# Optimization experiments

Measured on AMD Instinct MI355X. Metric: run time of the kernel, lower is better.

## Reference

```python
import jax, jax.numpy as jnp
import numpy as np

N_HEADS = 16
HEAD_SIZE = 64
SEQ_LEN = 2048
EMBED = 1024
BATCH = 2


def setup_inputs() -> dict:
    key = jax.random.key(0)
    ks = jax.random.split(key, 9)
    d_inner = N_HEADS * HEAD_SIZE
    s = 1.0 / np.sqrt(EMBED)
    inp = {
        "inputs": jax.random.normal(ks[0], (BATCH, SEQ_LEN, EMBED), jnp.float32),
        "Wq": jax.random.uniform(ks[1], (EMBED, d_inner), jnp.float32, -s, s),
        "bq": jax.random.uniform(ks[2], (d_inner,), jnp.float32, -s, s),
        "Wk": jax.random.uniform(ks[3], (EMBED, d_inner), jnp.float32, -s, s),
        "bk": jax.random.uniform(ks[4], (d_inner,), jnp.float32, -s, s),
        "Wv": jax.random.uniform(ks[5], (EMBED, d_inner), jnp.float32, -s, s),
        "bv": jax.random.uniform(ks[6], (d_inner,), jnp.float32, -s, s),
        "Wo": jax.random.uniform(ks[7], (d_inner, EMBED), jnp.float32, -s, s),
        "bo": jax.random.uniform(ks[8], (EMBED,), jnp.float32, -s, s),
    }
    return inp


def reference(inputs, Wq, bq, Wk, bk, Wv, bv, Wo, bo):
    B, S, _ = inputs.shape
    # QKV projections -> [B, H, S, Dh]
    def proj(W, b):
        return (inputs @ W + b).reshape(B, S, N_HEADS, HEAD_SIZE).transpose(0, 2, 1, 3)
    q, k, v = proj(Wq, bq), proj(Wk, bk), proj(Wv, bv)
    scores = jnp.einsum("bhqd,bhkd->bhqk", q, k) / jnp.sqrt(jnp.float32(HEAD_SIZE))
    causal = jnp.tril(jnp.ones((S, S), dtype=bool))  # [S, S]
    scores = jnp.where(causal[None, None], scores, -jnp.inf)
    attn = jax.nn.softmax(scores, axis=-1)  # dropout is identity in eval
    out = jnp.einsum("bhqk,bhkd->bhqd", attn, v)
    out = out.transpose(0, 2, 1, 3).reshape(B, S, N_HEADS * HEAD_SIZE)
    return out @ Wo + bo
```

## Files before the change

kernel.cpp:

```cpp
#include <hip/hip_runtime.h>
#include <hip/hip_bf16.h>
#include <math.h>

#define NH 16
#define DH 64
#define SEQ 2048
#define EMBED 1024
#define DINNER 1024
#define BATCH 2
#define MTOK 4096

typedef __bf16 bf16x8 __attribute__((ext_vector_type(8)));
typedef float  f32x4  __attribute__((ext_vector_type(4)));
typedef float  f32x16 __attribute__((ext_vector_type(16)));
typedef unsigned int u32;

__device__ __forceinline__ void gload16(const void* g, void* l) {
    __builtin_amdgcn_global_load_lds((const __attribute__((address_space(1))) void*)g,
                                     (__attribute__((address_space(3))) void*)l, 16, 0, 0);
}

__global__ __launch_bounds__(256) void cvt_bf16(
    const float* __restrict__ src, __bf16* __restrict__ dst, int n)
{
    int i = (blockIdx.x * 256 + threadIdx.x) * 4;
    if (i + 3 < n) {
        float4 v = *(const float4*)&src[i];
        dst[i + 0] = (__bf16)v.x;
        dst[i + 1] = (__bf16)v.y;
        dst[i + 2] = (__bf16)v.z;
        dst[i + 3] = (__bf16)v.w;
    }
}

__global__ __launch_bounds__(256) void tconv4(
    const float* __restrict__ W0, const float* __restrict__ W1,
    const float* __restrict__ W2, const float* __restrict__ W3,
    __bf16* __restrict__ D0, __bf16* __restrict__ D1,
    __bf16* __restrict__ D2, __bf16* __restrict__ D3)
{
    const int z = blockIdx.z;
    const float* __restrict__ src = (z == 0) ? W0 : (z == 1) ? W1 : (z == 2) ? W2 : W3;
    __bf16* __restrict__ dst      = (z == 0) ? D0 : (z == 1) ? D1 : (z == 2) ? D2 : D3;
    const int R = 1024, C = 1024;

    __shared__ float t[32][33];
    const int c0 = blockIdx.x * 32, r0 = blockIdx.y * 32;
    const int x = threadIdx.x & 31, y = threadIdx.x >> 5;
#pragma unroll
    for (int i = 0; i < 4; ++i)
        t[y + 8 * i][x] = src[(size_t)(r0 + y + 8 * i) * C + c0 + x];
    __syncthreads();
#pragma unroll
    for (int i = 0; i < 4; ++i)
        dst[(size_t)(c0 + y + 8 * i) * R + r0 + x] = (__bf16)t[x][y + 8 * i];
}

#define QSCALE 0.18033688f

__global__ __launch_bounds__(512) void gemm128(
    const __bf16* __restrict__ A,
    const __bf16* __restrict__ Bt0, const __bf16* __restrict__ Bt1, const __bf16* __restrict__ Bt2,
    const float* __restrict__ b0, const float* __restrict__ b1, const float* __restrict__ b2,
    void* __restrict__ o0, void* __restrict__ o1, void* __restrict__ o2,
    int Kdim, int mode3)
{
    const int z = blockIdx.z;
    const __bf16* __restrict__ Bt = (z == 0) ? Bt0 : (z == 1) ? Bt1 : Bt2;
    const float*  __restrict__ bias = (z == 0) ? b0 : (z == 1) ? b1 : b2;
    void* __restrict__ outp = (z == 0) ? o0 : (z == 1) ? o1 : o2;
    const int mode = mode3 ? 3 : z;

    __shared__ __bf16 As[128 * 32];
    __shared__ __bf16 Bs[128 * 32];

    const int tid  = threadIdx.x;
    const int lane = tid & 63;
    const int wid  = tid >> 6;
    const int wm = wid >> 1, wn = wid & 1;
    const int ls = lane & 15, lg = lane >> 4;
    const int m0 = blockIdx.y * 128, n0 = blockIdx.x * 128;

    const int sr = tid >> 2;
    const int sc = (tid & 3) * 8;

    f32x4 acc[2][4] = {};

    for (int k0 = 0; k0 < Kdim; k0 += 32) {
        gload16(&A [(size_t)(m0 + sr) * Kdim + k0 + sc], &As[sr * 32 + sc]);
        gload16(&Bt[(size_t)(n0 + sr) * Kdim + k0 + sc], &Bs[sr * 32 + sc]);
        __syncthreads();

        bf16x8 af[2], bfr[4];
#pragma unroll
        for (int i = 0; i < 2; ++i)
            af[i] = *(const bf16x8*)&As[(wm * 32 + i * 16 + ls) * 32 + lg * 8];
#pragma unroll
        for (int jx = 0; jx < 4; ++jx)
            bfr[jx] = *(const bf16x8*)&Bs[(wn * 64 + jx * 16 + ls) * 32 + lg * 8];
#pragma unroll
        for (int i = 0; i < 2; ++i)
#pragma unroll
            for (int jx = 0; jx < 4; ++jx)
                acc[i][jx] = __builtin_amdgcn_mfma_f32_16x16x32_bf16(af[i], bfr[jx], acc[i][jx], 0, 0, 0);
        __syncthreads();
    }

#pragma unroll
    for (int i = 0; i < 2; ++i) {
#pragma unroll
        for (int jx = 0; jx < 4; ++jx) {
            const int mbase = m0 + wm * 32 + i * 16 + lg * 4;
            const int n = n0 + wn * 64 + jx * 16 + ls;
            if (mode == 3) {
#pragma unroll
                for (int j = 0; j < 4; ++j)
                    ((float*)outp)[(size_t)(mbase + j) * EMBED + n] = acc[i][jx][j] + bias[n];
            } else if (mode == 2) {
                const int b = mbase >> 11, s = mbase & 2047;
                const int h = n >> 6, d = n & 63;
                __bf16 t4[4];
#pragma unroll
                for (int j = 0; j < 4; ++j) t4[j] = (__bf16)(acc[i][jx][j] + bias[n]);
                *(uint2*)&((__bf16*)outp)[(((size_t)(b * NH + h) * DH + d) << 11) + s] = *(uint2*)t4;
            } else {
                const float sc2 = (mode == 0) ? QSCALE : 1.0f;
#pragma unroll
                for (int j = 0; j < 4; ++j) {
                    const int m = mbase + j;
                    const int b = m >> 11, s = m & 2047;
                    const int h = n >> 6, d = n & 63;
                    ((__bf16*)outp)[((((size_t)(b * NH + h) << 11) + s) * DH) + d] =
                        (__bf16)((acc[i][jx][j] + bias[n]) * sc2);
                }
            }
        }
    }
}

__global__ __launch_bounds__(64) void attn_mfma(
    const __bf16* __restrict__ Q, const __bf16* __restrict__ K,
    const __bf16* __restrict__ Vt, __bf16* __restrict__ ctx)
{
    __shared__ __bf16 lds[12288];

    const int lane = threadIdx.x & 63;
    const int col  = lane & 31;
    const int hi   = lane >> 5;
    const int bh   = blockIdx.x & 31;
    const int qt32 = 63 - (blockIdx.x >> 5);
    const int qlo  = qt32 * 32;
    const int b = bh >> 4, h = bh & 15;

    const __bf16* __restrict__ Qb = Q + ((size_t)bh << 11) * DH;
    const char* __restrict__ Kg = (const char*)(K  + ((size_t)bh << 11) * DH);
    const char* __restrict__ Vg = (const char*)(Vt + ((size_t)bh << 11) * DH);

    char* const ldsK0 = (char*)&lds[0];
    char* const ldsV  = ldsK0 + 16384;

    const int srow = lane >> 3;
    const int sswz = ((lane & 7) * 16) ^ (srow << 4);
    const int swz  = (col & 7) << 4;

    bf16x8 qf[4];
#pragma unroll
    for (int c = 0; c < 4; ++c)
        qf[c] = *(const bf16x8*)&Qb[(size_t)(qlo + col) * DH + c * 16 + hi * 8];

    const int nt = (qt32 + 2) >> 1;

#pragma unroll
    for (int i = 0; i < 8; ++i)
        gload16(Kg + (size_t)(i * 8 + srow) * 128 + sswz, ldsK0 + i * 1024 + lane * 16);
#pragma unroll
    for (int i = 0; i < 8; ++i)
        gload16(Vg + (size_t)(i * 8 + srow) * 4096 + sswz, ldsV + i * 1024 + lane * 16);
    if (nt > 1) {
#pragma unroll
        for (int i = 0; i < 8; ++i)
            gload16(Kg + (size_t)(64 + i * 8 + srow) * 128 + sswz,
                    ldsK0 + 8192 + i * 1024 + lane * 16);
    }

    f32x16 oT0 = {}, oT1 = {};
    float mrun = 0.f, lrun = 0.f;

    for (int t = 0; t < nt; ++t) {
        const int k0 = t * 64;
        const char* ldsK = ldsK0 + (t & 1) * 8192;
        const bool haveK1 = (t + 1 < nt);
        const bool stageK2 = (t + 2 < nt);

        if (haveK1) { asm volatile("s_waitcnt vmcnt(16)" ::: "memory"); }
        else        { asm volatile("s_waitcnt vmcnt(8)"  ::: "memory"); }

        bf16x8 kfa[4], kfb[4];
#pragma unroll
        for (int c = 0; c < 4; ++c) {
            kfa[c] = *(const bf16x8*)(ldsK + (     col) * 128 + ((c * 32 + hi * 16) ^ swz));
            kfb[c] = *(const bf16x8*)(ldsK + (32 + col) * 128 + ((c * 32 + hi * 16) ^ swz));
        }

        __builtin_amdgcn_s_setprio(1);
        f32x16 sta = {}, stb = {};
#pragma unroll
        for (int c = 0; c < 4; ++c) {
            sta = __builtin_amdgcn_mfma_f32_32x32x16_bf16(kfa[c], qf[c], sta, 0, 0, 0);
            stb = __builtin_amdgcn_mfma_f32_32x32x16_bf16(kfb[c], qf[c], stb, 0, 0, 0);
        }
        __builtin_amdgcn_s_setprio(0);

        asm volatile("s_waitcnt lgkmcnt(0)" ::: "memory");
        __builtin_amdgcn_sched_barrier(0);
        if (stageK2) {
            const int kbn = (t + 2) * 64;
#pragma unroll
            for (int i = 0; i < 8; ++i)
                gload16(Kg + (size_t)(kbn + i * 8 + srow) * 128 + sswz,
                        ldsK0 + (t & 1) * 8192 + i * 1024 + lane * 16);
        }

        if (k0 + 63 > qlo) {
#pragma unroll
            for (int r = 0; r < 16; ++r) {
                const int krel = (r & 3) + 8 * (r >> 2) + 4 * hi;
                if (k0 + krel > qlo + col)      sta[r] = -INFINITY;
                if (k0 + 32 + krel > qlo + col) stb[r] = -INFINITY;
            }
        }

        if (t == 0) {
            float ta = fmaxf(fmaxf(fmaxf(sta[0], sta[1]), fmaxf(sta[2], sta[3])),
                             fmaxf(fmaxf(sta[4], sta[5]), fmaxf(sta[6], sta[7])));
            float tb = fmaxf(fmaxf(fmaxf(sta[8], sta[9]),  fmaxf(sta[10], sta[11])),
                             fmaxf(fmaxf(sta[12], sta[13]), fmaxf(sta[14], sta[15])));
            float tc = fmaxf(fmaxf(fmaxf(stb[0], stb[1]), fmaxf(stb[2], stb[3])),
                             fmaxf(fmaxf(stb[4], stb[5]), fmaxf(stb[6], stb[7])));
            float td = fmaxf(fmaxf(fmaxf(stb[8], stb[9]),  fmaxf(stb[10], stb[11])),
                             fmaxf(fmaxf(stb[12], stb[13]), fmaxf(stb[14], stb[15])));
            float tmax = fmaxf(fmaxf(ta, tb), fmaxf(tc, td));
            tmax = fmaxf(tmax, __shfl_xor(tmax, 32));
            mrun = tmax;
        }

        float pa[16], pb[16];
#pragma unroll
        for (int r = 0; r < 16; ++r) { pa[r] = exp2f(sta[r] - mrun); pb[r] = exp2f(stb[r] - mrun); }
        float psa = (((pa[0] + pa[1]) + (pa[2] + pa[3])) + ((pa[4] + pa[5]) + (pa[6] + pa[7])))
                  + (((pa[8] + pa[9]) + (pa[10] + pa[11])) + ((pa[12] + pa[13]) + (pa[14] + pa[15])));
        float psb = (((pb[0] + pb[1]) + (pb[2] + pb[3])) + ((pb[4] + pb[5]) + (pb[6] + pb[7])))
                  + (((pb[8] + pb[9]) + (pb[10] + pb[11])) + ((pb[12] + pb[13]) + (pb[14] + pb[15])));
        float psum = psa + psb;
        psum += __shfl_xor(psum, 32);
        lrun += psum;

        u32 wa[8], wb[8];
#pragma unroll
        for (int i = 0; i < 8; ++i) {
            u32 r1, r2;
            asm("v_cvt_pk_bf16_f32 %0, %1, %2" : "=v"(r1) : "v"(pa[2 * i]), "v"(pa[2 * i + 1]));
            asm("v_cvt_pk_bf16_f32 %0, %1, %2" : "=v"(r2) : "v"(pb[2 * i]), "v"(pb[2 * i + 1]));
            wa[i] = r1; wb[i] = r2;
        }
        asm("v_permlane32_swap_b32 %0, %1" : "+v"(wa[0]), "+v"(wa[2]));
        asm("v_permlane32_swap_b32 %0, %1" : "+v"(wa[1]), "+v"(wa[3]));
        asm("v_permlane32_swap_b32 %0, %1" : "+v"(wa[4]), "+v"(wa[6]));
        asm("v_permlane32_swap_b32 %0, %1" : "+v"(wa[5]), "+v"(wa[7]));
        asm("v_permlane32_swap_b32 %0, %1" : "+v"(wb[0]), "+v"(wb[2]));
        asm("v_permlane32_swap_b32 %0, %1" : "+v"(wb[1]), "+v"(wb[3]));
        asm("v_permlane32_swap_b32 %0, %1" : "+v"(wb[4]), "+v"(wb[6]));
        asm("v_permlane32_swap_b32 %0, %1" : "+v"(wb[5]), "+v"(wb[7]));

        union { u32 u4[4]; bf16x8 v; } cA0, cA1, cB0, cB1;
        cA0.u4[0] = wa[0]; cA0.u4[1] = wa[1]; cA0.u4[2] = wa[2]; cA0.u4[3] = wa[3];
        cA1.u4[0] = wa[4]; cA1.u4[1] = wa[5]; cA1.u4[2] = wa[6]; cA1.u4[3] = wa[7];
        cB0.u4[0] = wb[0]; cB0.u4[1] = wb[1]; cB0.u4[2] = wb[2]; cB0.u4[3] = wb[3];
        cB1.u4[0] = wb[4]; cB1.u4[1] = wb[5]; cB1.u4[2] = wb[6]; cB1.u4[3] = wb[7];

        if (stageK2)      { asm volatile("s_waitcnt vmcnt(16)" ::: "memory"); }
        else if (haveK1)  { asm volatile("s_waitcnt vmcnt(8)"  ::: "memory"); }
        else              { asm volatile("s_waitcnt vmcnt(0)"  ::: "memory"); }

        __builtin_amdgcn_s_setprio(1);
#pragma unroll
        for (int dh = 0; dh < 2; ++dh) {
            bf16x8 v0 = *(const bf16x8*)(ldsV + (dh * 32 + col) * 128 + ((0  + hi * 16) ^ swz));
            bf16x8 v1 = *(const bf16x8*)(ldsV + (dh * 32 + col) * 128 + ((32 + hi * 16) ^ swz));
            bf16x8 v2 = *(const bf16x8*)(ldsV + (dh * 32 + col) * 128 + ((64 + hi * 16) ^ swz));
            bf16x8 v3 = *(const bf16x8*)(ldsV + (dh * 32 + col) * 128 + ((96 + hi * 16) ^ swz));
            f32x16& o = dh ? oT1 : oT0;
            o = __builtin_amdgcn_mfma_f32_32x32x16_bf16(v0, cA0.v, o, 0, 0, 0);
            o = __builtin_amdgcn_mfma_f32_32x32x16_bf16(v1, cA1.v, o, 0, 0, 0);
            o = __builtin_amdgcn_mfma_f32_32x32x16_bf16(v2, cB0.v, o, 0, 0, 0);
            o = __builtin_amdgcn_mfma_f32_32x32x16_bf16(v3, cB1.v, o, 0, 0, 0);
        }
        __builtin_amdgcn_s_setprio(0);

        asm volatile("s_waitcnt lgkmcnt(0)" ::: "memory");
        __builtin_amdgcn_sched_barrier(0);
        if (haveK1) {
            const int kbn = (t + 1) * 64;
#pragma unroll
            for (int i = 0; i < 8; ++i)
                gload16(Vg + (size_t)(i * 8 + srow) * 4096 + (size_t)kbn * 2 + sswz,
                        ldsV + i * 1024 + lane * 16);
        }
    }

    const float inv = 1.0f / lrun;
    const size_t base = ((size_t)(b * SEQ + qlo + col)) * DINNER + h * 64;
#pragma unroll
    for (int g = 0; g < 4; ++g) {
        __bf16 t4[4];
#pragma unroll
        for (int j = 0; j < 4; ++j) t4[j] = (__bf16)(oT0[4 * g + j] * inv);
        *(uint2*)&ctx[base + 8 * g + 4 * hi] = *(uint2*)t4;
#pragma unroll
        for (int j = 0; j < 4; ++j) t4[j] = (__bf16)(oT1[4 * g + j] * inv);
        *(uint2*)&ctx[base + 32 + 8 * g + 4 * hi] = *(uint2*)t4;
    }
}

extern "C" void kernel_launch(void* const* d_in, const int* in_sizes, int n_in,
                              void* d_out, int out_size, void* d_ws, size_t ws_size,
                              hipStream_t stream)
{
    const float* X  = (const float*)d_in[0];
    const float* Wq = (const float*)d_in[1];
    const float* bq = (const float*)d_in[2];
    const float* Wk = (const float*)d_in[3];
    const float* bk = (const float*)d_in[4];
    const float* Wv = (const float*)d_in[5];
    const float* bv = (const float*)d_in[6];
    const float* Wo = (const float*)d_in[7];
    const float* bo = (const float*)d_in[8];
    float* out = (float*)d_out;

    __bf16* ws  = (__bf16*)d_ws;
    const size_t MI = 1048576;
    __bf16* Xb   = ws;
    __bf16* Wtq  = ws + 4  * MI;
    __bf16* Wtk  = ws + 5  * MI;
    __bf16* Wtv  = ws + 6  * MI;
    __bf16* Wto  = ws + 7  * MI;
    __bf16* Qb   = ws + 8  * MI;
    __bf16* Kb   = ws + 12 * MI;
    __bf16* Vtb  = ws + 16 * MI;
    __bf16* ctxb = ws + 20 * MI;

    cvt_bf16<<<dim3(MTOK * EMBED / 1024), dim3(256), 0, stream>>>(X, Xb, MTOK * EMBED);
    tconv4<<<dim3(32, 32, 4), dim3(256), 0, stream>>>(Wq, Wk, Wv, Wo, Wtq, Wtk, Wtv, Wto);

    {
        dim3 grid(DINNER / 128, MTOK / 128, 3), blk(512);
        gemm128<<<grid, blk, 0, stream>>>(Xb, Wtq, Wtk, Wtv, bq, bk, bv,
                                          Qb, Kb, Vtb, EMBED, 0);
    }

    {
        dim3 grid(32 * (SEQ / 32)), blk(64);
        attn_mfma<<<grid, blk, 0, stream>>>(Qb, Kb, Vtb, ctxb);
    }

    {
        dim3 grid(EMBED / 128, MTOK / 128, 1), blk(512);
        gemm128<<<grid, blk, 0, stream>>>(ctxb, Wto, Wto, Wto, bo, bo, bo,
                                          out, out, out, DINNER, 1);
    }
}
```

Baseline: 125.4 us.

## Load V tiles straight from global into registers instead of staging through LDS

The attention kernel no longer copies V tiles into LDS with async global-to-LDS loads. Each lane now reads its V fragments directly from global memory into registers, and the loop prefetches the next tile's fragments one iteration ahead. This removes the LDS writes and reads for V, the explicit vmcnt/lgkmcnt waits around V, and a third of the shared-memory footprint, which may allow more resident waves. In exchange, the per-lane global reads use a large row stride, which may coalesce poorly. The compiler's automatic waits for these register loads may also serialize behind the in-flight K prefetches, reducing overlap.

```diff
diff --git a/kernel.cpp b/kernel.cpp
--- a/kernel.cpp
+++ b/kernel.cpp
@@ -142,7 +142,7 @@
     const __bf16* __restrict__ Q, const __bf16* __restrict__ K,
     const __bf16* __restrict__ Vt, __bf16* __restrict__ ctx)
 {
-    __shared__ __bf16 lds[12288];
+    __shared__ __bf16 lds[8192];
 
     const int lane = threadIdx.x & 63;
     const int col  = lane & 31;
@@ -157,12 +157,14 @@
     const char* __restrict__ Vg = (const char*)(Vt + ((size_t)bh << 11) * DH);
 
     char* const ldsK0 = (char*)&lds[0];
-    char* const ldsV  = ldsK0 + 16384;
 
     const int srow = lane >> 3;
     const int sswz = ((lane & 7) * 16) ^ (srow << 4);
     const int swz  = (col & 7) << 4;
 
+    const int vbase0 = (     col) * 4096 + hi * 16;
+    const int vbase1 = (32 + col) * 4096 + hi * 16;
+
     bf16x8 qf[4];
 #pragma unroll
     for (int c = 0; c < 4; ++c)
@@ -173,15 +175,21 @@
 #pragma unroll
     for (int i = 0; i < 8; ++i)
         gload16(Kg + (size_t)(i * 8 + srow) * 128 + sswz, ldsK0 + i * 1024 + lane * 16);
-#pragma unroll
-    for (int i = 0; i < 8; ++i)
-        gload16(Vg + (size_t)(i * 8 + srow) * 4096 + sswz, ldsV + i * 1024 + lane * 16);
     if (nt > 1) {
 #pragma unroll
         for (int i = 0; i < 8; ++i)
             gload16(Kg + (size_t)(64 + i * 8 + srow) * 128 + sswz,
                     ldsK0 + 8192 + i * 1024 + lane * 16);
     }
+    bf16x8 v0a, v1a, v2a, v3a, v0b, v1b, v2b, v3b;
+    v0a = *(const bf16x8*)(Vg + vbase0);
+    v1a = *(const bf16x8*)(Vg + vbase0 + 32);
+    v2a = *(const bf16x8*)(Vg + vbase0 + 64);
+    v3a = *(const bf16x8*)(Vg + vbase0 + 96);
+    v0b = *(const bf16x8*)(Vg + vbase1);
+    v1b = *(const bf16x8*)(Vg + vbase1 + 32);
+    v2b = *(const bf16x8*)(Vg + vbase1 + 64);
+    v3b = *(const bf16x8*)(Vg + vbase1 + 96);
 
     f32x16 oT0 = {}, oT1 = {};
     float mrun = 0.f, lrun = 0.f;
@@ -220,6 +228,20 @@
                 gload16(Kg + (size_t)(kbn + i * 8 + srow) * 128 + sswz,
                         ldsK0 + (t & 1) * 8192 + i * 1024 + lane * 16);
         }
+
+        bf16x8 n0a, n1a, n2a, n3a, n0b, n1b, n2b, n3b;
+        if (haveK1) {
+            const int vb = (t + 1) * 128;
+            n0a = *(const bf16x8*)(Vg + vbase0 + vb);
+            n1a = *(const bf16x8*)(Vg + vbase0 + vb + 32);
+            n2a = *(const bf16x8*)(Vg + vbase0 + vb + 64);
+            n3a = *(const bf16x8*)(Vg + vbase0 + vb + 96);
+            n0b = *(const bf16x8*)(Vg + vbase1 + vb);
+            n1b = *(const bf16x8*)(Vg + vbase1 + vb + 32);
+            n2b = *(const bf16x8*)(Vg + vbase1 + vb + 64);
+            n3b = *(const bf16x8*)(Vg + vbase1 + vb + 96);
+        }
+        __builtin_amdgcn_sched_barrier(0);
 
         if (k0 + 63 > qlo) {
 #pragma unroll
@@ -278,33 +300,20 @@
         cB0.u4[0] = wb[0]; cB0.u4[1] = wb[1]; cB0.u4[2] = wb[2]; cB0.u4[3] = wb[3];
         cB1.u4[0] = wb[4]; cB1.u4[1] = wb[5]; cB1.u4[2] = wb[6]; cB1.u4[3] = wb[7];
 
-        if (stageK2)      { asm volatile("s_waitcnt vmcnt(16)" ::: "memory"); }
-        else if (haveK1)  { asm volatile("s_waitcnt vmcnt(8)"  ::: "memory"); }
-        else              { asm volatile("s_waitcnt vmcnt(0)"  ::: "memory"); }
-
         __builtin_amdgcn_s_setprio(1);
-#pragma unroll
-        for (int dh = 0; dh < 2; ++dh) {
-            bf16x8 v0 = *(const bf16x8*)(ldsV + (dh * 32 + col) * 128 + ((0  + hi * 16) ^ swz));
-            bf16x8 v1 = *(const bf16x8*)(ldsV + (dh * 32 + col) * 128 + ((32 + hi * 16) ^ swz));
-            bf16x8 v2 = *(const bf16x8*)(ldsV + (dh * 32 + col) * 128 + ((64 + hi * 16) ^ swz));
-            bf16x8 v3 = *(const bf16x8*)(ldsV + (dh * 32 + col) * 128 + ((96 + hi * 16) ^ swz));
-            f32x16& o = dh ? oT1 : oT0;
-            o = __builtin_amdgcn_mfma_f32_32x32x16_bf16(v0, cA0.v, o, 0, 0, 0);
-            o = __builtin_amdgcn_mfma_f32_32x32x16_bf16(v1, cA1.v, o, 0, 0, 0);
-            o = __builtin_amdgcn_mfma_f32_32x32x16_bf16(v2, cB0.v, o, 0, 0, 0);
-            o = __builtin_amdgcn_mfma_f32_32x32x16_bf16(v3, cB1.v, o, 0, 0, 0);
-        }
+        oT0 = __builtin_amdgcn_mfma_f32_32x32x16_bf16(v0a, cA0.v, oT0, 0, 0, 0);
+        oT0 = __builtin_amdgcn_mfma_f32_32x32x16_bf16(v1a, cA1.v, oT0, 0, 0, 0);
+        oT0 = __builtin_amdgcn_mfma_f32_32x32x16_bf16(v2a, cB0.v, oT0, 0, 0, 0);
+        oT0 = __builtin_amdgcn_mfma_f32_32x32x16_bf16(v3a, cB1.v, oT0, 0, 0, 0);
+        oT1 = __builtin_amdgcn_mfma_f32_32x32x16_bf16(v0b, cA0.v, oT1, 0, 0, 0);
+        oT1 = __builtin_amdgcn_mfma_f32_32x32x16_bf16(v1b, cA1.v, oT1, 0, 0, 0);
+        oT1 = __builtin_amdgcn_mfma_f32_32x32x16_bf16(v2b, cB0.v, oT1, 0, 0, 0);
+        oT1 = __builtin_amdgcn_mfma_f32_32x32x16_bf16(v3b, cB1.v, oT1, 0, 0, 0);
         __builtin_amdgcn_s_setprio(0);
 
-        asm volatile("s_waitcnt lgkmcnt(0)" ::: "memory");
-        __builtin_amdgcn_sched_barrier(0);
         if (haveK1) {
-            const int kbn = (t + 1) * 64;
-#pragma unroll
-            for (int i = 0; i < 8; ++i)
-                gload16(Vg + (size_t)(i * 8 + srow) * 4096 + (size_t)kbn * 2 + sswz,
-                        ldsV + i * 1024 + lane * 16);
+            v0a = n0a; v1a = n1a; v2a = n2a; v3a = n3a;
+            v0b = n0b; v1b = n1b; v2b = n2b; v3b = n3b;
         }
     }
 
```

Result: slower. 130.4 us (+4.0%).
